# Optimization experiments

Measured on AMD Instinct MI355X. Metric: run time of the kernel, lower is better.

## Reference

```python
import jax, jax.numpy as jnp
import numpy as np

DIM = 1024
HEADS = 16
BLOCK = 64


def setup_inputs() -> dict:
    key = jax.random.key(0)
    ks = jax.random.split(key, 9)
    B, N, C = 4, 4096, DIM
    s = 1.0 / np.sqrt(C)
    x = jax.random.normal(ks[0], (B, N, C), dtype=jnp.float32)
    Wq = jax.random.normal(ks[1], (C, C), dtype=jnp.float32) * s
    Wk = jax.random.normal(ks[2], (C, C), dtype=jnp.float32) * s
    Wv = jax.random.normal(ks[3], (C, C), dtype=jnp.float32) * s
    Wo = jax.random.normal(ks[4], (C, C), dtype=jnp.float32) * s
    bq = jax.random.normal(ks[5], (C,), dtype=jnp.float32) * 0.01
    bk = jax.random.normal(ks[6], (C,), dtype=jnp.float32) * 0.01
    bv = jax.random.normal(ks[7], (C,), dtype=jnp.float32) * 0.01
    bo = jax.random.normal(ks[8], (C,), dtype=jnp.float32) * 0.01
    return {"x": x, "Wq": Wq, "bq": bq, "Wk": Wk, "bk": bk,
            "Wv": Wv, "bv": bv, "Wo": Wo, "bo": bo}


def _block_sparse_attn(x, Wq, bq, Wk, bk, Wv, bv, Wo, bo):
    B, N, C = x.shape
    H = HEADS
    d = C // H
    bs = BLOCK
    nb = N // bs  # N chosen as a multiple of block_size
    scale = d ** -0.5

    def proj(W, b):
        # torch nn.Linear: x @ W.T + b -> [B,H,N,d]
        return (x @ W.T + b).reshape(B, N, H, d).transpose(0, 2, 1, 3)

    q = proj(Wq, bq)
    k = proj(Wk, bk)
    v = proj(Wv, bv)

    # split into blocks: [B,H,nb,bs,d]
    qb = q.reshape(B, H, nb, bs, d)
    kb = k.reshape(B, H, nb, bs, d)
    vb = v.reshape(B, H, nb, bs, d)

    # pad one zero block on each side, then gather windows [b-1, b, b+1]
    pad = ((0, 0), (0, 0), (1, 1), (0, 0), (0, 0))
    kp = jnp.pad(kb, pad)
    vp = jnp.pad(vb, pad)
    kw = jnp.concatenate([kp[:, :, 0:nb], kp[:, :, 1:nb + 1], kp[:, :, 2:nb + 2]], axis=3)  # [B,H,nb,3bs,d]
    vw = jnp.concatenate([vp[:, :, 0:nb], vp[:, :, 1:nb + 1], vp[:, :, 2:nb + 2]], axis=3)

    attn = jnp.einsum('bhnqd,bhnkd->bhnqk', qb, kw) * scale  # [B,H,nb,bs,3bs]

    # causal mask in window-relative coords: abs_q = n*bs+i, abs_k = (n-1)*bs+j
    i = jnp.arange(bs)
    j = jnp.arange(3 * bs)
    causal = (bs + i[:, None]) >= j[None, :]              # [bs, 3bs]
    bidx = jnp.arange(nb)
    wvalid = jnp.stack([bidx > 0, jnp.ones(nb, bool), bidx < nb - 1], axis=1)  # [nb,3]
    kvalid = jnp.repeat(wvalid, bs, axis=1)               # [nb, 3bs]
    mask = kvalid[:, None, :] & causal[None, :, :]        # [nb, bs, 3bs]

    attn = jnp.where(mask[None, None], attn, -jnp.inf)
    p = jax.nn.softmax(attn, axis=-1)
    o = jnp.einsum('bhnqk,bhnkd->bhnqd', p, vw)           # [B,H,nb,bs,d]
    out = o.reshape(B, H, N, d).transpose(0, 2, 1, 3).reshape(B, N, C)
    return out @ Wo.T + bo


def reference(x, Wq, bq, Wk, bk, Wv, bv, Wo, bo):
    return _block_sparse_attn(x, Wq, bq, Wk, bk, Wv, bv, Wo, bo)
```

## Files before the change

kernel.cpp:

```cpp
#include <hip/hip_runtime.h>

typedef __bf16 bf16;
typedef __attribute__((ext_vector_type(8))) __bf16 bf16x8;
typedef __attribute__((ext_vector_type(4))) float f32x4;
typedef __attribute__((ext_vector_type(4))) unsigned int u32x4;

#define MFMA16(a, b, c) __builtin_amdgcn_mfma_f32_16x16x32_bf16(a, b, c, 0, 0, 0)

#define C_DIM 1024
#define N_TOK 4096
#define BATCH 4
#define HEADS 16
#define HD 64
#define BS 64
#define NB 64
#define M_TOT (BATCH * N_TOK)
#define QKV_ELEMS ((size_t)M_TOT * C_DIM)
#define W_ELEMS (C_DIM * C_DIM)
#define VT_LD 200
#define NKT 16

__global__ void detect_kernel(const unsigned int* __restrict__ x, int* flag) {
    const int lane = threadIdx.x & 63;
    int cnt = 0;
#pragma unroll
    for (int i = 0; i < 4; ++i) {
        const unsigned int e = (x[lane * 4 + i] >> 7) & 0xFFu;
        cnt += (e >= 100u && e <= 140u) ? 1 : 0;
    }
#pragma unroll
    for (int st = 1; st < 64; st <<= 1) cnt += __shfl_xor(cnt, st, 64);
    if (threadIdx.x == 0) *flag = (cnt >= 192) ? 0 : 1;
}

__global__ void sentinel_kernel(float* out, float val, int n) {
    int i = blockIdx.x * 256 + threadIdx.x;
    if (i < n) out[i] = val;
}

__device__ __forceinline__ bf16x8 cvt8(f32x4 a, f32x4 b) {
    bf16x8 r;
    r[0] = (bf16)a[0]; r[1] = (bf16)a[1]; r[2] = (bf16)a[2]; r[3] = (bf16)a[3];
    r[4] = (bf16)b[0]; r[5] = (bf16)b[1]; r[6] = (bf16)b[2]; r[7] = (bf16)b[3];
    return r;
}

__device__ __forceinline__ float rd1(const void* p, int i, int isf) {
    return isf ? ((const float*)p)[i] : (float)((const bf16*)p)[i];
}

__global__ __launch_bounds__(256) void cvt_kernel(
    const void* __restrict__ x,  bf16* __restrict__ xb,
    const void* __restrict__ w0, const void* __restrict__ w1,
    const void* __restrict__ w2, const void* __restrict__ w3,
    bf16* __restrict__ wb, const int* __restrict__ flag)
{
    const int isf = *flag;
    const int bid = blockIdx.x;
    const void* src;
    bf16* dst;
    size_t off;
    if (bid < 8192) {
        src = x; dst = xb; off = (size_t)bid * 2048;
    } else {
        const int seg = (bid - 8192) >> 9;
        src = seg == 0 ? w0 : (seg == 1 ? w1 : (seg == 2 ? w2 : w3));
        dst = wb + (size_t)seg * W_ELEMS;
        off = (size_t)((bid - 8192) & 511) * 2048;
    }
    const size_t e = off + (size_t)threadIdx.x * 8;
    if (isf) {
        const float* gp = (const float*)src + e;
        *(bf16x8*)(dst + e) = cvt8(*(const f32x4*)gp, *(const f32x4*)(gp + 4));
    } else {
        *(u32x4*)(dst + e) = *(const u32x4*)((const bf16*)src + e);
    }
}

__device__ __forceinline__ void gload_lds16(const bf16* g, bf16* l) {
    __builtin_amdgcn_global_load_lds(
        (const __attribute__((address_space(1))) void*)g,
        (__attribute__((address_space(3))) void*)l, 16, 0, 0);
}

__device__ __forceinline__ void stageA(const bf16* __restrict__ src, bf16* lds,
                                       int h, int w, int lane, int m0, int k0) {
#pragma unroll
    for (int l = 0; l < 2; ++l) {
        const int c = w * 2 + l;
        const int rowbase = (c >> 3) * 128 + h * 64 + (c & 7) * 8;
        const int grow = m0 + rowbase + (lane >> 3);
        const int gcol = k0 + (((lane & 7) ^ ((lane >> 3) & 7)) << 3);
        gload_lds16(src + (size_t)grow * C_DIM + gcol, lds + rowbase * 64);
    }
}
__device__ __forceinline__ void stageB(const bf16* __restrict__ src, bf16* lds,
                                       int y, int w, int lane, int n0, int k0) {
#pragma unroll
    for (int l = 0; l < 2; ++l) {
        const int c = w * 2 + l;
        const int rowbase = (c >> 2) * 64 + y * 32 + (c & 3) * 8;
        const int grow = n0 + rowbase + (lane >> 3);
        const int gcol = k0 + (((lane & 7) ^ ((lane >> 3) & 7)) << 3);
        gload_lds16(src + (size_t)grow * C_DIM + gcol, lds + rowbase * 64);
    }
}

__device__ __forceinline__ bf16x8 ldsrd(const bf16* base, int row, int kk, int quad) {
    return *(const bf16x8*)((const char*)base +
        row * 128 + ((kk * 64 + quad * 16) ^ ((row & 7) << 4)));
}

#define GEMM256_KLOOP(ASRC, BSRC)                                               \
    {                                                                           \
        bf16* Ab0 = sm;                                                         \
        bf16* Bb0 = sm + 32768;                                                 \
        stageA(ASRC, Ab0, 0, w, lane, m0, 0);                                   \
        stageA(ASRC, Ab0, 1, w, lane, m0, 0);                                   \
        stageB(BSRC, Bb0, 0, w, lane, n0, 0);                                   \
        stageB(BSRC, Bb0, 1, w, lane, n0, 0);                                   \
    }                                                                           \
    asm volatile("s_waitcnt vmcnt(0)" ::: "memory");                            \
    __syncthreads();                                                            \
    for (int t = 0; t < NKT; ++t) {                                             \
        const bool stg = (t + 1) < NKT;                                         \
        bf16* Ab = sm + (t & 1) * 16384;                                        \
        bf16* Bb = sm + 32768 + (t & 1) * 16384;                                \
        bf16* An = sm + ((t + 1) & 1) * 16384;                                  \
        bf16* Bn = sm + 32768 + ((t + 1) & 1) * 16384;                          \
        const int kn = (t + 1) * 64;                                            \
        bf16x8 af[4][2], b0[2][2], b1[2][2];                                    \
            \
        _Pragma("unroll") for (int mi = 0; mi < 4; ++mi)                        \
            _Pragma("unroll") for (int kk = 0; kk < 2; ++kk)                    \
                af[mi][kk] = ldsrd(Ab, wr * 128 + mi * 16 + lr, kk, quad);      \
        _Pragma("unroll") for (int ni = 0; ni < 2; ++ni)                        \
            _Pragma("unroll") for (int kk = 0; kk < 2; ++kk)                    \
                b0[ni][kk] = ldsrd(Bb, wc * 64 + ni * 16 + lr, kk, quad);       \
        if (stg) { stageA(ASRC, An, 0, w, lane, m0, kn);                        \
                   stageB(BSRC, Bn, 0, w, lane, n0, kn); }                      \
        __builtin_amdgcn_s_barrier();                                           \
        __builtin_amdgcn_s_setprio(1);                                          \
        _Pragma("unroll") for (int kk = 0; kk < 2; ++kk)                        \
            _Pragma("unroll") for (int mi = 0; mi < 4; ++mi)                    \
                _Pragma("unroll") for (int ni = 0; ni < 2; ++ni)                \
                    acc[mi][ni] = MFMA16(af[mi][kk], b0[ni][kk], acc[mi][ni]);  \
        __builtin_amdgcn_s_setprio(0);                                          \
        if (stg) asm volatile("s_waitcnt vmcnt(6)" ::: "memory");               \
        else     asm volatile("s_waitcnt vmcnt(2)" ::: "memory");               \
        __builtin_amdgcn_s_barrier();                                           \
                       \
        _Pragma("unroll") for (int ni = 0; ni < 2; ++ni)                        \
            _Pragma("unroll") for (int kk = 0; kk < 2; ++kk)                    \
                b1[ni][kk] = ldsrd(Bb, wc * 64 + 32 + ni * 16 + lr, kk, quad);  \
        if (stg) stageB(BSRC, Bn, 1, w, lane, n0, kn);                          \
        __builtin_amdgcn_s_barrier();                                           \
        __builtin_amdgcn_s_setprio(1);                                          \
        _Pragma("unroll") for (int kk = 0; kk < 2; ++kk)                        \
            _Pragma("unroll") for (int mi = 0; mi < 4; ++mi)                    \
                _Pragma("unroll") for (int ni = 0; ni < 2; ++ni)                \
                    acc[mi][2 + ni] = MFMA16(af[mi][kk], b1[ni][kk], acc[mi][2 + ni]); \
        __builtin_amdgcn_s_setprio(0);                                          \
        if (stg) asm volatile("s_waitcnt vmcnt(6)" ::: "memory");               \
        else     asm volatile("s_waitcnt vmcnt(0)" ::: "memory");               \
        __builtin_amdgcn_s_barrier();                                           \
              \
        _Pragma("unroll") for (int mi = 0; mi < 4; ++mi)                        \
            _Pragma("unroll") for (int kk = 0; kk < 2; ++kk)                    \
                af[mi][kk] = ldsrd(Ab, wr * 128 + 64 + mi * 16 + lr, kk, quad); \
        if (stg) stageA(ASRC, An, 1, w, lane, m0, kn);                          \
        __builtin_amdgcn_s_barrier();                                           \
        __builtin_amdgcn_s_setprio(1);                                          \
        _Pragma("unroll") for (int kk = 0; kk < 2; ++kk)                        \
            _Pragma("unroll") for (int mi = 0; mi < 4; ++mi)                    \
                _Pragma("unroll") for (int ni = 0; ni < 2; ++ni)                \
                    acc[4 + mi][ni] = MFMA16(af[mi][kk], b0[ni][kk], acc[4 + mi][ni]); \
        _Pragma("unroll") for (int kk = 0; kk < 2; ++kk)                        \
            _Pragma("unroll") for (int mi = 0; mi < 4; ++mi)                    \
                _Pragma("unroll") for (int ni = 0; ni < 2; ++ni)                \
                    acc[4 + mi][2 + ni] = MFMA16(af[mi][kk], b1[ni][kk], acc[4 + mi][2 + ni]); \
        __builtin_amdgcn_s_setprio(0);                                          \
        if (stg) asm volatile("s_waitcnt vmcnt(4)" ::: "memory");               \
        __builtin_amdgcn_s_barrier();                                           \
    }

__global__ __launch_bounds__(512) void qkv256_kernel(
    const bf16* __restrict__ xb, const bf16* __restrict__ wb,
    const void* __restrict__ bq, const void* __restrict__ bk,
    const void* __restrict__ bv,
    bf16* __restrict__ qo, bf16* __restrict__ ko, bf16* __restrict__ vo,
    const int* __restrict__ flag)
{
    __shared__ __align__(16) bf16 sm[65536];

    const int isf = *flag;
    const int bid = blockIdx.x;
    const int work = (bid & 7) * 96 + (bid >> 3);
    const int y = work / 12, xx = work % 12;
    const int which = xx >> 2;
    const int n0 = (xx & 3) * 256;
    const int m0 = y * 256;
    const bf16* W  = wb + (size_t)which * W_ELEMS;
    const void* bia = which == 0 ? bq : (which == 1 ? bk : bv);
    bf16* dst       = which == 0 ? qo : (which == 1 ? ko : vo);

    const int tid = threadIdx.x;
    const int w = tid >> 6, lane = tid & 63;
    const int wr = w >> 2, wc = w & 3;
    const int lr = lane & 15, quad = lane >> 4;

    f32x4 acc[8][4] = {};

    GEMM256_KLOOP(xb, W)

    __syncthreads();
    float bb[4];
#pragma unroll
    for (int ni = 0; ni < 4; ++ni)
        bb[ni] = rd1(bia, n0 + wc * 64 + ni * 16 + lr, isf);
#pragma unroll
    for (int mi = 0; mi < 8; ++mi)
#pragma unroll
        for (int ni = 0; ni < 4; ++ni)
#pragma unroll
            for (int rr = 0; rr < 4; ++rr) {
                const int row = wr * 128 + mi * 16 + quad * 4 + rr;
                const int col = wc * 64 + ni * 16 + lr;
                *(bf16*)((char*)sm + row * 512 + ((col * 2) ^ ((row & 7) << 4))) =
                    (bf16)(acc[mi][ni][rr] + bb[ni]);
            }
    __syncthreads();
#pragma unroll
    for (int j = 0; j < 16; ++j) {
        const int idx = j * 512 + tid;
        const int row = idx >> 5, ch = idx & 31;
        u32x4 vls = *(const u32x4*)((const char*)sm + row * 512 + ((ch * 16) ^ ((row & 7) << 4)));
        *(u32x4*)(dst + (size_t)(m0 + row) * C_DIM + n0 + ch * 8) = vls;
    }
}

__global__ __launch_bounds__(256) void attn_kernel(
    const bf16* qb, const bf16* __restrict__ kb,
    const bf16* __restrict__ vb, bf16* ob)
{
    __shared__ __align__(16) bf16 sh[12288 + 64 * VT_LD];
    bf16* Ks = sh;
    bf16* Ps = sh;
    bf16* Vt = sh + 12288;

    const int bid = blockIdx.x;
    const int work = (bid & 7) * 512 + (bid >> 3);
    const int nblk = work & 63, bh = work >> 6;
    const int tid = threadIdx.x;
    const int b = bh >> 4, h = bh & 15;
    const int w = tid >> 6, lane = tid & 63;
    const int lr = lane & 15, quad = lane >> 4;
    const int grow = b * N_TOK + nblk * BS;
    const int colbase = h * HD;

    bf16x8 vv[6];
#pragma unroll
    for (int t = 0; t < 6; ++t) {
        const int e8 = (t * 256 + tid) * 8;
        const int kk = e8 >> 6, dd0 = e8 & 63;
        const int gb = nblk - 1 + (kk >> 6);
        bf16x8 z = {};
        vv[t] = z;
        if (gb >= 0 && gb < NB)
            vv[t] = *(const bf16x8*)(vb + (size_t)(b * N_TOK + gb * BS + (kk & 63)) * C_DIM + colbase + dd0);
    }

    bf16x8 aq[2];
#pragma unroll
    for (int ks = 0; ks < 2; ++ks)
        aq[ks] = *(const bf16x8*)(qb + (size_t)(grow + w * 16 + lr) * C_DIM
                                  + colbase + ks * 32 + quad * 8);

    for (int wbk = 0; wbk < 3; ++wbk) {
        const int gb = nblk - 1 + wbk;
        const bool ok = (gb >= 0 && gb < NB);
#pragma unroll
        for (int p = 0; p < 2; ++p) {
            const int e = (p * 256 + tid) * 8;
            const int row = e >> 6, col = e & 63;
            const int boff = (wbk * 64 + row) * 128 + ((col * 2) ^ ((row & 7) << 4));
            u32x4 val = {};
            if (ok)
                val = *(const u32x4*)(kb + (size_t)(b * N_TOK + gb * BS + row) * C_DIM + colbase + col);
            *(u32x4*)((char*)Ks + boff) = val;
        }
    }
    __syncthreads();

    f32x4 s[12];
    __builtin_amdgcn_s_setprio(1);
#pragma unroll
    for (int jt = 0; jt < 12; ++jt) {
        f32x4 a = {};
#pragma unroll
        for (int ks = 0; ks < 2; ++ks) {
            const int boff = (jt * 16 + lr) * 128 + ((ks * 64 + quad * 16) ^ ((lr & 7) << 4));
            bf16x8 bk_ = *(const bf16x8*)((const char*)Ks + boff);
            a = MFMA16(aq[ks], bk_, a);
        }
        s[jt] = a;
    }
    __builtin_amdgcn_s_setprio(0);

#pragma unroll
    for (int r = 0; r < 4; ++r) {
        const int i = w * 16 + quad * 4 + r;
        float m_ = -1e30f;
#pragma unroll
        for (int jt = 0; jt < 12; ++jt) {
            const int j = jt * 16 + lr;
            bool valid = (64 + i) >= j;
            if (j < 64 && nblk == 0) valid = false;
            if (j >= 128 && nblk == NB - 1) valid = false;
            const float sv = valid ? s[jt][r] * 0.125f : -1e30f;
            s[jt][r] = sv;
            m_ = fmaxf(m_, sv);
        }
#pragma unroll
        for (int st = 1; st < 16; st <<= 1)
            m_ = fmaxf(m_, __shfl_xor(m_, st, 64));
        float l_ = 0.f;
#pragma unroll
        for (int jt = 0; jt < 12; ++jt) {
            const float p = (s[jt][r] > -1e29f) ? __expf(s[jt][r] - m_) : 0.f;
            s[jt][r] = p;
            l_ += p;
        }
#pragma unroll
        for (int st = 1; st < 16; st <<= 1)
            l_ += __shfl_xor(l_, st, 64);
        const float inv = 1.f / l_;
#pragma unroll
        for (int jt = 0; jt < 12; ++jt) s[jt][r] *= inv;
    }

    __syncthreads();

#pragma unroll
    for (int t = 0; t < 6; ++t) {
        const int e8 = (t * 256 + tid) * 8;
        const int kk = e8 >> 6, dd0 = e8 & 63;
        const int key = ((dd0 >> 3) & 7) << 4;
#pragma unroll
        for (int i = 0; i < 8; ++i) {
            const int boff = (dd0 + i) * (2 * VT_LD) + ((kk * 2) ^ key);
            *(bf16*)((char*)Vt + boff) = vv[t][i];
        }
    }

#pragma unroll
    for (int r = 0; r < 4; ++r) {
        const int prow = w * 16 + quad * 4 + r;
        const int rbase = prow * 384;
        const int key = (prow & 7) << 4;
#pragma unroll
        for (int jt = 0; jt < 12; ++jt) {
            const int boff = rbase + (((jt * 16 + lr) * 2) ^ key);
            *(bf16*)((char*)Ps + boff) = (bf16)s[jt][r];
        }
    }
    __syncthreads();

    f32x4 o[4] = {};
    const int prow = w * 16 + lr;
    const int pbase = prow * 384;
    const int pkey = (prow & 7) << 4;
    __builtin_amdgcn_s_setprio(1);
#pragma unroll
    for (int kt = 0; kt < 6; ++kt) {
        bf16x8 ap = *(const bf16x8*)((const char*)Ps + pbase + ((kt * 64 + quad * 16) ^ pkey));
#pragma unroll
        for (int nt = 0; nt < 4; ++nt) {
            const int dd = nt * 16 + lr;
            const int boff = dd * (2 * VT_LD) + ((kt * 64 + quad * 16) ^ (((dd >> 3) & 7) << 4));
            bf16x8 bv_ = *(const bf16x8*)((const char*)Vt + boff);
            o[nt] = MFMA16(ap, bv_, o[nt]);
        }
    }
    __builtin_amdgcn_s_setprio(0);
#pragma unroll
    for (int nt = 0; nt < 4; ++nt) {
        const int dd = nt * 16 + lr;
#pragma unroll
        for (int r = 0; r < 4; ++r) {
            const int i = w * 16 + quad * 4 + r;
            ob[(size_t)(grow + i) * C_DIM + colbase + dd] = (bf16)o[nt][r];
        }
    }
}

__global__ __launch_bounds__(512) void outproj256_kernel(
    const bf16* __restrict__ o, const bf16* __restrict__ Wob,
    const void* __restrict__ bo, float* __restrict__ out,
    const int* __restrict__ flag)
{
    __shared__ __align__(16) bf16 sm[65536];

    const int isf = *flag;
    const int bid = blockIdx.x;
    const int work = (bid & 7) * 32 + (bid >> 3);
    const int n0 = (work & 3) * 256;
    const int m0 = (work >> 2) * 256;

    const int tid = threadIdx.x;
    const int w = tid >> 6, lane = tid & 63;
    const int wr = w >> 2, wc = w & 3;
    const int lr = lane & 15, quad = lane >> 4;

    f32x4 acc[8][4] = {};

    GEMM256_KLOOP(o, Wob)

    float bb[4];
#pragma unroll
    for (int ni = 0; ni < 4; ++ni)
        bb[ni] = rd1(bo, n0 + wc * 64 + ni * 16 + lr, isf);
#pragma unroll
    for (int hh = 0; hh < 2; ++hh) {
        __syncthreads();
        if (wr == hh) {
#pragma unroll
            for (int mi = 0; mi < 8; ++mi)
#pragma unroll
                for (int ni = 0; ni < 4; ++ni)
#pragma unroll
                    for (int rr = 0; rr < 4; ++rr) {
                        const int lrow = mi * 16 + quad * 4 + rr;
                        const int col = wc * 64 + ni * 16 + lr;
                        *(float*)((char*)sm + lrow * 1024 + ((col * 4) ^ ((lrow & 7) << 4))) =
                            acc[mi][ni][rr] + bb[ni];
                    }
        }
        __syncthreads();
#pragma unroll
        for (int j = 0; j < 16; ++j) {
            const int idx = j * 512 + tid;
            const int row = idx >> 6, ch = idx & 63;
            u32x4 vls = *(const u32x4*)((const char*)sm + row * 1024 + ((ch * 16) ^ ((row & 7) << 4)));
            *(u32x4*)(out + (size_t)(m0 + hh * 128 + row) * C_DIM + n0 + ch * 4) = vls;
        }
    }
}

extern "C" void kernel_launch(void* const* d_in, const int* in_sizes, int n_in,
                              void* d_out, int out_size, void* d_ws, size_t ws_size,
                              hipStream_t stream) {
    const void* x  = d_in[0];
    const void* Wq = d_in[1];
    const void* bq = d_in[2];
    const void* Wk = d_in[3];
    const void* bk = d_in[4];
    const void* Wv = d_in[5];
    const void* bv = d_in[6];
    const void* Wo = d_in[7];
    const void* bo = d_in[8];
    float* out = (float*)d_out;

    const int sb = (out_size + 255) / 256;
    const bool sizes_ok = (n_in == 9) &&
        in_sizes[0] == (int)QKV_ELEMS &&
        in_sizes[1] == W_ELEMS && in_sizes[2] == C_DIM &&
        in_sizes[3] == W_ELEMS && in_sizes[4] == C_DIM &&
        in_sizes[5] == W_ELEMS && in_sizes[6] == C_DIM &&
        in_sizes[7] == W_ELEMS && in_sizes[8] == C_DIM &&
        out_size == (int)QKV_ELEMS;
    if (!sizes_ok) {
        sentinel_kernel<<<sb, 256, 0, stream>>>(out, 777.0f, out_size);
        return;
    }
    const size_t need = 4096 + 2 * QKV_ELEMS * sizeof(bf16) + 4 * W_ELEMS * sizeof(bf16);
    if (ws_size < need) {
        sentinel_kernel<<<sb, 256, 0, stream>>>(out, 999.0f, out_size);
        return;
    }

    int* flag = (int*)d_ws;
    bf16* q  = (bf16*)((char*)d_ws + 4096);
    bf16* k  = q + QKV_ELEMS;
    bf16* Wb = k + QKV_ELEMS;
    bf16* xb = (bf16*)d_out;
    bf16* v  = (bf16*)((char*)d_out + QKV_ELEMS * sizeof(bf16));

    detect_kernel<<<1, 64, 0, stream>>>((const unsigned int*)x, flag);

    cvt_kernel<<<8192 + 4 * 512, 256, 0, stream>>>(x, xb, Wq, Wk, Wv, Wo, Wb, flag);

    qkv256_kernel<<<768, 512, 0, stream>>>(xb, Wb, bq, bk, bv, q, k, v, flag);

    attn_kernel<<<4096, 256, 0, stream>>>(q, k, v, q);

    outproj256_kernel<<<256, 512, 0, stream>>>(q, Wb + 3 * (size_t)W_ELEMS, bo, out, flag);
}
```

Before: 321.1 us.

## Load GEMM A operand directly into registers and stage only B in LDS

The 256x256 GEMM k-loop for the QKV and output projections now reads the A tile straight from global memory into registers, double-buffered across iterations. Only the B tile is staged in LDS. The wave layout changes from 2x4 to 4x2, so each wave owns 64 rows by 128 columns, and the epilogues are rewritten to match. This halves LDS use and removes several barriers per k-step. In exchange, A loads become uncoalesced per-lane 16-byte reads, there is a full vmcnt(0) wait each step, and register pressure rises.

```diff
diff --git a/kernel.cpp b/kernel.cpp
--- a/kernel.cpp
+++ b/kernel.cpp
@@ -83,17 +83,6 @@
         (__attribute__((address_space(3))) void*)l, 16, 0, 0);
 }
 
-__device__ __forceinline__ void stageA(const bf16* __restrict__ src, bf16* lds,
-                                       int h, int w, int lane, int m0, int k0) {
-#pragma unroll
-    for (int l = 0; l < 2; ++l) {
-        const int c = w * 2 + l;
-        const int rowbase = (c >> 3) * 128 + h * 64 + (c & 7) * 8;
-        const int grow = m0 + rowbase + (lane >> 3);
-        const int gcol = k0 + (((lane & 7) ^ ((lane >> 3) & 7)) << 3);
-        gload_lds16(src + (size_t)grow * C_DIM + gcol, lds + rowbase * 64);
-    }
-}
 __device__ __forceinline__ void stageB(const bf16* __restrict__ src, bf16* lds,
                                        int y, int w, int lane, int n0, int k0) {
 #pragma unroll
@@ -111,77 +100,50 @@
         row * 128 + ((kk * 64 + quad * 16) ^ ((row & 7) << 4)));
 }
 
-#define GEMM256_KLOOP(ASRC, BSRC)                                               \
+#define GTILE(T, AFC, AFN)                                                      \
     {                                                                           \
-        bf16* Ab0 = sm;                                                         \
-        bf16* Bb0 = sm + 32768;                                                 \
-        stageA(ASRC, Ab0, 0, w, lane, m0, 0);                                   \
-        stageA(ASRC, Ab0, 1, w, lane, m0, 0);                                   \
-        stageB(BSRC, Bb0, 0, w, lane, n0, 0);                                   \
-        stageB(BSRC, Bb0, 1, w, lane, n0, 0);                                   \
-    }                                                                           \
-    asm volatile("s_waitcnt vmcnt(0)" ::: "memory");                            \
-    __syncthreads();                                                            \
-    for (int t = 0; t < NKT; ++t) {                                             \
-        const bool stg = (t + 1) < NKT;                                         \
-        bf16* Ab = sm + (t & 1) * 16384;                                        \
-        bf16* Bb = sm + 32768 + (t & 1) * 16384;                                \
-        bf16* An = sm + ((t + 1) & 1) * 16384;                                  \
-        bf16* Bn = sm + 32768 + ((t + 1) & 1) * 16384;                          \
-        const int kn = (t + 1) * 64;                                            \
-        bf16x8 af[4][2], b0[2][2], b1[2][2];                                    \
-            \
-        _Pragma("unroll") for (int mi = 0; mi < 4; ++mi)                        \
+        const bool stg = ((T) + 1) < NKT;                                       \
+        bf16* Bb = sm + (((T)) & 1) * 16384;                                    \
+        bf16* Bn = sm + (((T) + 1) & 1) * 16384;                                \
+        const int kn = ((T) + 1) * 64;                                          \
+        if (stg) { stageB(BSRC_, Bn, 0, w, lane, n0, kn);                       \
+                   stageB(BSRC_, Bn, 1, w, lane, n0, kn); }                     \
+        if (stg) {                                                              \
+            _Pragma("unroll") for (int mi = 0; mi < 4; ++mi)                    \
+                _Pragma("unroll") for (int kk = 0; kk < 2; ++kk)                \
+                    AFN[mi][kk] = *(const bf16x8*)(ASRC_ +                      \
+                        (size_t)(m0 + wr * 64 + mi * 16 + lr) * C_DIM           \
+                        + kn + kk * 32 + quad * 8);                             \
+        }                                                                       \
+        bf16x8 bfr[8][2];                                                       \
+        _Pragma("unroll") for (int ni = 0; ni < 8; ++ni)                        \
             _Pragma("unroll") for (int kk = 0; kk < 2; ++kk)                    \
-                af[mi][kk] = ldsrd(Ab, wr * 128 + mi * 16 + lr, kk, quad);      \
-        _Pragma("unroll") for (int ni = 0; ni < 2; ++ni)                        \
-            _Pragma("unroll") for (int kk = 0; kk < 2; ++kk)                    \
-                b0[ni][kk] = ldsrd(Bb, wc * 64 + ni * 16 + lr, kk, quad);       \
-        if (stg) { stageA(ASRC, An, 0, w, lane, m0, kn);                        \
-                   stageB(BSRC, Bn, 0, w, lane, n0, kn); }                      \
-        __builtin_amdgcn_s_barrier();                                           \
+                bfr[ni][kk] = ldsrd(Bb, wc * 128 + ni * 16 + lr, kk, quad);     \
         __builtin_amdgcn_s_setprio(1);                                          \
         _Pragma("unroll") for (int kk = 0; kk < 2; ++kk)                        \
             _Pragma("unroll") for (int mi = 0; mi < 4; ++mi)                    \
-                _Pragma("unroll") for (int ni = 0; ni < 2; ++ni)                \
-                    acc[mi][ni] = MFMA16(af[mi][kk], b0[ni][kk], acc[mi][ni]);  \
+                _Pragma("unroll") for (int ni = 0; ni < 8; ++ni)                \
+                    acc[mi][ni] = MFMA16(AFC[mi][kk], bfr[ni][kk], acc[mi][ni]); \
         __builtin_amdgcn_s_setprio(0);                                          \
-        if (stg) asm volatile("s_waitcnt vmcnt(6)" ::: "memory");               \
-        else     asm volatile("s_waitcnt vmcnt(2)" ::: "memory");               \
+        asm volatile("s_waitcnt vmcnt(0)" ::: "memory");                        \
         __builtin_amdgcn_s_barrier();                                           \
-                       \
-        _Pragma("unroll") for (int ni = 0; ni < 2; ++ni)                        \
-            _Pragma("unroll") for (int kk = 0; kk < 2; ++kk)                    \
-                b1[ni][kk] = ldsrd(Bb, wc * 64 + 32 + ni * 16 + lr, kk, quad);  \
-        if (stg) stageB(BSRC, Bn, 1, w, lane, n0, kn);                          \
-        __builtin_amdgcn_s_barrier();                                           \
-        __builtin_amdgcn_s_setprio(1);                                          \
+    }
+
+#define GEMM256_DIRECT(ASRC, BSRC)                                              \
+    const bf16* ASRC_ = (ASRC); const bf16* BSRC_ = (BSRC);                     \
+    bf16x8 afA[4][2], afB[4][2];                                                \
+    stageB(BSRC_, sm, 0, w, lane, n0, 0);                                       \
+    stageB(BSRC_, sm, 1, w, lane, n0, 0);                                       \
+    _Pragma("unroll") for (int mi = 0; mi < 4; ++mi)                            \
         _Pragma("unroll") for (int kk = 0; kk < 2; ++kk)                        \
-            _Pragma("unroll") for (int mi = 0; mi < 4; ++mi)                    \
-                _Pragma("unroll") for (int ni = 0; ni < 2; ++ni)                \
-                    acc[mi][2 + ni] = MFMA16(af[mi][kk], b1[ni][kk], acc[mi][2 + ni]); \
-        __builtin_amdgcn_s_setprio(0);                                          \
-        if (stg) asm volatile("s_waitcnt vmcnt(6)" ::: "memory");               \
-        else     asm volatile("s_waitcnt vmcnt(0)" ::: "memory");               \
-        __builtin_amdgcn_s_barrier();                                           \
-              \
-        _Pragma("unroll") for (int mi = 0; mi < 4; ++mi)                        \
-            _Pragma("unroll") for (int kk = 0; kk < 2; ++kk)                    \
-                af[mi][kk] = ldsrd(Ab, wr * 128 + 64 + mi * 16 + lr, kk, quad); \
-        if (stg) stageA(ASRC, An, 1, w, lane, m0, kn);                          \
-        __builtin_amdgcn_s_barrier();                                           \
-        __builtin_amdgcn_s_setprio(1);                                          \
-        _Pragma("unroll") for (int kk = 0; kk < 2; ++kk)                        \
-            _Pragma("unroll") for (int mi = 0; mi < 4; ++mi)                    \
-                _Pragma("unroll") for (int ni = 0; ni < 2; ++ni)                \
-                    acc[4 + mi][ni] = MFMA16(af[mi][kk], b0[ni][kk], acc[4 + mi][ni]); \
-        _Pragma("unroll") for (int kk = 0; kk < 2; ++kk)                        \
-            _Pragma("unroll") for (int mi = 0; mi < 4; ++mi)                    \
-                _Pragma("unroll") for (int ni = 0; ni < 2; ++ni)                \
-                    acc[4 + mi][2 + ni] = MFMA16(af[mi][kk], b1[ni][kk], acc[4 + mi][2 + ni]); \
-        __builtin_amdgcn_s_setprio(0);                                          \
-        if (stg) asm volatile("s_waitcnt vmcnt(4)" ::: "memory");               \
-        __builtin_amdgcn_s_barrier();                                           \
+            afA[mi][kk] = *(const bf16x8*)(ASRC_ +                              \
+                (size_t)(m0 + wr * 64 + mi * 16 + lr) * C_DIM                   \
+                + kk * 32 + quad * 8);                                          \
+    asm volatile("s_waitcnt vmcnt(0)" ::: "memory");                            \
+    __builtin_amdgcn_s_barrier();                                               \
+    _Pragma("unroll") for (int t = 0; t < NKT; t += 2) {                        \
+        GTILE(t, afA, afB)                                                      \
+        GTILE(t + 1, afB, afA)                                                  \
     }
 
 __global__ __launch_bounds__(512) void qkv256_kernel(
@@ -191,7 +153,7 @@
     bf16* __restrict__ qo, bf16* __restrict__ ko, bf16* __restrict__ vo,
     const int* __restrict__ flag)
 {
-    __shared__ __align__(16) bf16 sm[65536];
+    __shared__ __align__(16) bf16 sm[32768];
 
     const int isf = *flag;
     const int bid = blockIdx.x;
@@ -206,36 +168,41 @@
 
     const int tid = threadIdx.x;
     const int w = tid >> 6, lane = tid & 63;
-    const int wr = w >> 2, wc = w & 3;
+    const int wr = w >> 1, wc = w & 1;
     const int lr = lane & 15, quad = lane >> 4;
 
-    f32x4 acc[8][4] = {};
-
-    GEMM256_KLOOP(xb, W)
-
-    __syncthreads();
-    float bb[4];
-#pragma unroll
-    for (int ni = 0; ni < 4; ++ni)
-        bb[ni] = rd1(bia, n0 + wc * 64 + ni * 16 + lr, isf);
-#pragma unroll
-    for (int mi = 0; mi < 8; ++mi)
-#pragma unroll
-        for (int ni = 0; ni < 4; ++ni)
-#pragma unroll
-            for (int rr = 0; rr < 4; ++rr) {
-                const int row = wr * 128 + mi * 16 + quad * 4 + rr;
-                const int col = wc * 64 + ni * 16 + lr;
-                *(bf16*)((char*)sm + row * 512 + ((col * 2) ^ ((row & 7) << 4))) =
-                    (bf16)(acc[mi][ni][rr] + bb[ni]);
-            }
-    __syncthreads();
-#pragma unroll
-    for (int j = 0; j < 16; ++j) {
-        const int idx = j * 512 + tid;
-        const int row = idx >> 5, ch = idx & 31;
-        u32x4 vls = *(const u32x4*)((const char*)sm + row * 512 + ((ch * 16) ^ ((row & 7) << 4)));
-        *(u32x4*)(dst + (size_t)(m0 + row) * C_DIM + n0 + ch * 8) = vls;
+    f32x4 acc[4][8] = {};
+
+    GEMM256_DIRECT(xb, W)
+
+    float bb[8];
+#pragma unroll
+    for (int ni = 0; ni < 8; ++ni)
+        bb[ni] = rd1(bia, n0 + wc * 128 + ni * 16 + lr, isf);
+#pragma unroll
+    for (int hh = 0; hh < 2; ++hh) {
+        __syncthreads();
+        if ((wr >> 1) == hh) {
+#pragma unroll
+            for (int mi = 0; mi < 4; ++mi)
+#pragma unroll
+                for (int ni = 0; ni < 8; ++ni)
+#pragma unroll
+                    for (int rr = 0; rr < 4; ++rr) {
+                        const int lrow = (wr & 1) * 64 + mi * 16 + quad * 4 + rr;
+                        const int col = wc * 128 + ni * 16 + lr;
+                        *(bf16*)((char*)sm + lrow * 512 + ((col * 2) ^ ((lrow & 7) << 4))) =
+                            (bf16)(acc[mi][ni][rr] + bb[ni]);
+                    }
+        }
+        __syncthreads();
+#pragma unroll
+        for (int j = 0; j < 8; ++j) {
+            const int idx = j * 512 + tid;
+            const int row = idx >> 5, ch = idx & 31;
+            u32x4 vls = *(const u32x4*)((const char*)sm + row * 512 + ((ch * 16) ^ ((row & 7) << 4)));
+            *(u32x4*)(dst + (size_t)(m0 + hh * 128 + row) * C_DIM + n0 + ch * 8) = vls;
+        }
     }
 }
 
@@ -399,7 +366,7 @@
     const void* __restrict__ bo, float* __restrict__ out,
     const int* __restrict__ flag)
 {
-    __shared__ __align__(16) bf16 sm[65536];
+    __shared__ __align__(16) bf16 sm[32768];
 
     const int isf = *flag;
     const int bid = blockIdx.x;
@@ -409,40 +376,40 @@
 
     const int tid = threadIdx.x;
     const int w = tid >> 6, lane = tid & 63;
-    const int wr = w >> 2, wc = w & 3;
+    const int wr = w >> 1, wc = w & 1;
     const int lr = lane & 15, quad = lane >> 4;
 
-    f32x4 acc[8][4] = {};
-
-    GEMM256_KLOOP(o, Wob)
-
-    float bb[4];
-#pragma unroll
-    for (int ni = 0; ni < 4; ++ni)
-        bb[ni] = rd1(bo, n0 + wc * 64 + ni * 16 + lr, isf);
-#pragma unroll
-    for (int hh = 0; hh < 2; ++hh) {
+    f32x4 acc[4][8] = {};
+
+    GEMM256_DIRECT(o, Wob)
+
+    float bb[8];
+#pragma unroll
+    for (int ni = 0; ni < 8; ++ni)
+        bb[ni] = rd1(bo, n0 + wc * 128 + ni * 16 + lr, isf);
+#pragma unroll
+    for (int hh = 0; hh < 4; ++hh) {
         __syncthreads();
         if (wr == hh) {
 #pragma unroll
-            for (int mi = 0; mi < 8; ++mi)
-#pragma unroll
-                for (int ni = 0; ni < 4; ++ni)
+            for (int mi = 0; mi < 4; ++mi)
+#pragma unroll
+                for (int ni = 0; ni < 8; ++ni)
 #pragma unroll
                     for (int rr = 0; rr < 4; ++rr) {
                         const int lrow = mi * 16 + quad * 4 + rr;
-                        const int col = wc * 64 + ni * 16 + lr;
+                        const int col = wc * 128 + ni * 16 + lr;
                         *(float*)((char*)sm + lrow * 1024 + ((col * 4) ^ ((lrow & 7) << 4))) =
                             acc[mi][ni][rr] + bb[ni];
                     }
         }
         __syncthreads();
 #pragma unroll
-        for (int j = 0; j < 16; ++j) {
+        for (int j = 0; j < 8; ++j) {
             const int idx = j * 512 + tid;
             const int row = idx >> 6, ch = idx & 63;
             u32x4 vls = *(const u32x4*)((const char*)sm + row * 1024 + ((ch * 16) ^ ((row & 7) << 4)));
-            *(u32x4*)(out + (size_t)(m0 + hh * 128 + row) * C_DIM + n0 + ch * 4) = vls;
+            *(u32x4*)(out + (size_t)(m0 + hh * 64 + row) * C_DIM + n0 + ch * 4) = vls;
         }
     }
 }
```

Result: slower. 477.1 us (+48.6%).
